# Kernel optimization log

Hardware: AMD Instinct MI355X
Metric: run time of the kernel (lower is better)

The kernel has to match this reference:

```python
import jax, jax.numpy as jnp
import numpy as np
from jax import lax

T, B, H_IN, H_HID = 2048, 64, 256, 256


def _orth(key, shape):
    a = jax.random.normal(key, shape, jnp.float32)
    if shape[0] >= shape[1]:
        q, _ = jnp.linalg.qr(a)
    else:
        q, _ = jnp.linalg.qr(a.T)
        q = q.T
    return q[: shape[0], : shape[1]].astype(jnp.float32)


def setup_inputs() -> dict:
    key = jax.random.key(0)
    ks = jax.random.split(key, 6)
    x = jax.random.normal(ks[0], (T, B, H_IN), jnp.float32)
    rnn_hxs = jax.random.normal(ks[1], (1, B, H_HID), jnp.float32)
    batch_mask = jax.random.randint(ks[2], (T, B), 0, 2).astype(bool)
    # force column 0 fully valid so pad_packed max length == T (static shape)
    batch_mask = batch_mask.at[:, 0].set(True)
    w_ih = _orth(ks[3], (3 * H_HID, H_IN))   # [3H, H_in] gates r,z,n
    w_hh = _orth(ks[4], (3 * H_HID, H_HID))
    b_ih = jnp.zeros((3 * H_HID,), jnp.float32)  # constant_(0) init
    b_hh = jnp.zeros((3 * H_HID,), jnp.float32)
    return {"x": x, "rnn_hxs": rnn_hxs, "batch_mask": batch_mask,
            "w_ih": w_ih, "w_hh": w_hh, "b_ih": b_ih, "b_hh": b_hh}


def _gru_ragged(x, h0, batch_mask, w_ih, w_hh, b_ih, b_hh):
    Tn, Bn, _ = x.shape
    Hh = h0.shape[-1]
    mask = batch_mask
    lens = mask.sum(0)                      # [B] per-column valid lengths
    # --- gather/pack: move valid steps of each column to the front ---
    rank = jnp.cumsum(mask, axis=0) - mask  # compact position per (t,b)
    rank_m = jnp.where(mask, rank, Tn)      # invalid rows -> dump row Tn
    cols = jnp.broadcast_to(jnp.arange(Bn), (Tn, Bn))
    compact = jnp.zeros((Tn + 1, Bn, x.shape[-1]), x.dtype)
    compact = compact.at[rank_m, cols].set(x)[:Tn]
    # --- GRU over compact sequences; h frozen past each column's length ---
    gi = jnp.einsum('tbi,gi->tbg', compact, w_ih) + b_ih  # [T,B,3H]
    valid = jnp.arange(Tn)[:, None] < lens[None, :]       # [T,B]

    def step(h, inp):
        gi_t, v = inp
        gh = jnp.einsum('bh,gh->bg', h, w_hh) + b_hh
        r = jax.nn.sigmoid(gi_t[:, :Hh] + gh[:, :Hh])
        z = jax.nn.sigmoid(gi_t[:, Hh:2 * Hh] + gh[:, Hh:2 * Hh])
        n = jnp.tanh(gi_t[:, 2 * Hh:] + r * gh[:, 2 * Hh:])
        h_new = (1.0 - z) * n + z * h
        h_out = jnp.where(v[:, None], h_new, h)
        out = jnp.where(v[:, None], h_new, 0.0)  # pad_packed zero padding
        return h_out, out

    hT, scores = lax.scan(step, h0, (gi, valid))  # scores [T,B,Hh]
    # --- masked_scatter: true positions of dest (row-major t,b order)
    # consume consecutive H-rows of the flattened padded scores ---
    mflat = mask.reshape(-1)
    flat_rank = jnp.cumsum(mflat) - mflat            # exclusive cumsum
    src = scores.reshape(Tn * Bn, Hh)
    gathered = src[flat_rank]                        # [T*B, Hh]
    out = jnp.where(mflat[:, None], gathered, 0.0).reshape(Tn, Bn, Hh)
    return out, hT


def reference(x, rnn_hxs, batch_mask, w_ih, w_hh, b_ih, b_hh):
    scores, hT = _gru_ragged(x, rnn_hxs[0], batch_mask, w_ih, w_hh, b_ih, b_hh)
    return scores, hT[None]
```

## Files before the change

kernel.cpp:

```cpp
#include <hip/hip_runtime.h>
#include <cstdint>
#include <cstddef>

#define T_LEN 2048
#define B_N   64
#define H_INP 256
#define H_HID 256
#define G3    768
#define M_ROWS (T_LEN * B_N)
#define SCH   16

typedef _Float16 f16;
typedef _Float16 f16x2 __attribute__((ext_vector_type(2)));
typedef _Float16 f16x8 __attribute__((ext_vector_type(8)));
typedef float    f32x4 __attribute__((ext_vector_type(4)));

__global__ void k_zero(float4* __restrict__ p, int n4) {
  int i = blockIdx.x * blockDim.x + threadIdx.x;
  int stride = gridDim.x * blockDim.x;
  float4 z; z.x = z.y = z.z = z.w = 0.f;
  for (; i < n4; i += stride) p[i] = z;
}

__global__ void k_cvt(const float2* __restrict__ s, f16x2* __restrict__ d, int n2) {
  int i = blockIdx.x * blockDim.x + threadIdx.x;
  int stride = gridDim.x * blockDim.x;
  for (; i < n2; i += stride) {
    float2 v = s[i];
    f16x2 p; p.x = (f16)v.x; p.y = (f16)v.y;
    d[i] = p;
  }
}

__global__ __launch_bounds__(64) void k_prep_col(const int* __restrict__ mask,
                                                 unsigned short* __restrict__ tidx,
                                                 int* __restrict__ lens) {
  const int b = blockIdx.x;
  const int lane = threadIdx.x;
  unsigned short* tp = tidx + b * T_LEN;
  int base = 0;
  for (int c = 0; c < T_LEN / 64; ++c) {
    int t = c * 64 + lane;
    bool m = mask[t * B_N + b] != 0;
    unsigned long long bal = __ballot(m);
    int pc = __popcll(bal & ((1ull << lane) - 1ull));
    if (m) tp[base + pc] = (unsigned short)t;
    base += __popcll(bal);
  }
  if (lane == 0) lens[b] = base;
}

__global__ __launch_bounds__(256) void k_rowcnt(const int* __restrict__ mask,
                                                int* __restrict__ rowcnt) {
  int g = blockIdx.x * 256 + threadIdx.x;
  int t = g >> 6, lane = g & 63;
  bool m = mask[t * B_N + lane] != 0;
  unsigned long long bal = __ballot(m);
  if (lane == 0) rowcnt[t] = __popcll(bal);
}

__global__ __launch_bounds__(512) void k_rowpref(const int* __restrict__ rowcnt,
                                                 int* __restrict__ rowpref,
                                                 int* __restrict__ ntru) {
  const int tid = threadIdx.x;
  const int lane = tid & 63, w = tid >> 6;
  int4 v = ((const int4*)rowcnt)[tid];
  int s = v.x + v.y + v.z + v.w;
  int incl = s;
  for (int d = 1; d < 64; d <<= 1) {
    int t = __shfl_up(incl, d, 64);
    if (lane >= d) incl += t;
  }
  __shared__ int wt[8], wo[8];
  if (lane == 63) wt[w] = incl;
  __syncthreads();
  if (tid == 0) {
    int run = 0;
    for (int i = 0; i < 8; ++i) { wo[i] = run; run += wt[i]; }
    ntru[0] = run;
  }
  __syncthreads();
  int base = wo[w] + incl - s;
  int4 o; o.x = base; o.y = base + v.x; o.z = o.y + v.y; o.w = o.z + v.z;
  ((int4*)rowpref)[tid] = o;
}

__global__ __launch_bounds__(256) void k_inv(const int* __restrict__ mask,
                                             const int* __restrict__ rowpref,
                                             int* __restrict__ inv) {
  int g = blockIdx.x * 256 + threadIdx.x;
  int t = g >> 6, lane = g & 63;
  bool m = mask[t * B_N + lane] != 0;
  unsigned long long bal = __ballot(m);
  int r = rowpref[t] + __popcll(bal & ((1ull << lane) - 1ull));
  if (m) inv[r] = t * B_N + lane;
}

__global__ __launch_bounds__(256) void k_gemm(const f16* __restrict__ X,
                                              const f16* __restrict__ W,
                                              const float* __restrict__ bias,
                                              f16* __restrict__ GI) {
  const int lane = threadIdx.x & 63;
  const int wave = threadIdx.x >> 6;
  const int m0 = blockIdx.x * 64 + wave * 16;
  const int n0 = blockIdx.y * 64;
  const int idx16 = lane & 15;
  const int kofs  = (lane >> 4) * 8;

  const f16* ap  = X + (size_t)(m0 + idx16) * H_INP + kofs;
  const f16* bp0 = W + (size_t)(n0 + idx16) * H_INP + kofs;

  f32x4 acc[4] = { {0,0,0,0}, {0,0,0,0}, {0,0,0,0}, {0,0,0,0} };
#pragma unroll
  for (int kt = 0; kt < 8; ++kt) {
    f16x8 a = *(const f16x8*)(ap + kt * 32);
#pragma unroll
    for (int nt = 0; nt < 4; ++nt) {
      f16x8 bb = *(const f16x8*)(bp0 + (size_t)nt * 16 * H_INP + kt * 32);
      acc[nt] = __builtin_amdgcn_mfma_f32_16x16x32_f16(a, bb, acc[nt], 0, 0, 0);
    }
  }
  const int mbase = m0 + (lane >> 4) * 4;
#pragma unroll
  for (int nt = 0; nt < 4; ++nt) {
    const int col = n0 + nt * 16 + idx16;
    const float bv = bias[col];
#pragma unroll
    for (int r = 0; r < 4; ++r)
      GI[(size_t)(mbase + r) * G3 + col] = (f16)(acc[nt][r] + bv);
  }
}

__global__ __launch_bounds__(768) void k_scan(const f16* __restrict__ Whh,
                                              const f16* __restrict__ GI,
                                              const float* __restrict__ h0,
                                              const float* __restrict__ bhh,
                                              const unsigned short* __restrict__ tidx,
                                              const int* __restrict__ lens,
                                              const int* __restrict__ inv,
                                              const int* __restrict__ ntru,
                                              float* __restrict__ out) {
  const int b = blockIdx.x;
  const int tid = threadIdx.x;
  const int lane = tid & 63;
  const int wav = tid >> 6;

  __shared__ f16   GIbuf[SCH * G3];
  __shared__ float outb[SCH * H_HID];
  __shared__ float ghs[G3];
  __shared__ f16   hpk[H_HID];
  __shared__ int   ivb[2][SCH];

  f16x8 bf[4][8];
  {
    const f16* wbase = Whh + (size_t)(wav * 64 + (lane & 15)) * H_HID + ((lane >> 4) << 3);
#pragma unroll
    for (int nt = 0; nt < 4; ++nt)
#pragma unroll
      for (int kc = 0; kc < 8; ++kc)
        bf[nt][kc] = *(const f16x8*)(wbase + (size_t)nt * 16 * H_HID + kc * 32);
  }
  float br = 0.f, bz = 0.f, bn = 0.f, h_reg = 0.f;
  if (tid < H_HID) {
    br = bhh[tid]; bz = bhh[H_HID + tid]; bn = bhh[2 * H_HID + tid];
    h_reg = h0[b * H_HID + tid];
  }
  if (tid < H_HID / 2) {
    float2 hv = ((const float2*)(h0 + b * H_HID))[tid];
    f16x2 p; p.x = (f16)hv.x; p.y = (f16)hv.y;
    ((f16x2*)hpk)[tid] = p;
  }
  const int L  = lens[b];
  const int Nt = ntru[0];
  const unsigned short* tptr = tidx + b * T_LEN;
  const bool arow = (lane & 15) == 0;
  const int  q = lane >> 4;

  for (int k = 0; k < L; ++k) {
    if ((k & (SCH - 1)) == 0) {
      const int par = (k >> 4) & 1;
      if (k > 0) {
        for (int r = wav; r < SCH; r += 12) {
          int iv = ivb[par ^ 1][r];
          if (iv >= 0)
            *(float4*)(out + (size_t)iv * H_HID + (lane << 2)) =
                *(const float4*)(outb + r * H_HID + (lane << 2));
        }
      }
      {
        int nrows = L - k; if (nrows > SCH) nrows = SCH;
        int r = tid / 48, c = tid % 48;
        if (r < nrows) {
          int t = tptr[k + r];
          const uint4* src = (const uint4*)(GI + ((size_t)t * B_N + b) * G3) + (c << 1);
          uint4 v0 = src[0], v1 = src[1];
          uint4* dst = (uint4*)(GIbuf + r * G3) + (c << 1);
          dst[0] = v0; dst[1] = v1;
        }
        if (tid < SCH) {
          int kk = k + tid;
          int pr = kk * B_N + b;
          ivb[par][tid] = (kk < L && pr < Nt) ? inv[pr] : -1;
        }
      }
      __syncthreads();
    }
    {
      const f32x4 z4 = {0.f, 0.f, 0.f, 0.f};
      f16x8 af = {0, 0, 0, 0, 0, 0, 0, 0};
      if (arow) af = *(const f16x8*)(hpk + (q << 3));
      f32x4 a0 = __builtin_amdgcn_mfma_f32_16x16x32_f16(af, bf[0][0], z4, 0, 0, 0);
      f32x4 a1 = __builtin_amdgcn_mfma_f32_16x16x32_f16(af, bf[1][0], z4, 0, 0, 0);
      f32x4 a2 = __builtin_amdgcn_mfma_f32_16x16x32_f16(af, bf[2][0], z4, 0, 0, 0);
      f32x4 a3 = __builtin_amdgcn_mfma_f32_16x16x32_f16(af, bf[3][0], z4, 0, 0, 0);
#pragma unroll
      for (int kc = 1; kc < 8; ++kc) {
        f16x8 a = {0, 0, 0, 0, 0, 0, 0, 0};
        if (arow) a = *(const f16x8*)(hpk + kc * 32 + (q << 3));
        a0 = __builtin_amdgcn_mfma_f32_16x16x32_f16(a, bf[0][kc], a0, 0, 0, 0);
        a1 = __builtin_amdgcn_mfma_f32_16x16x32_f16(a, bf[1][kc], a1, 0, 0, 0);
        a2 = __builtin_amdgcn_mfma_f32_16x16x32_f16(a, bf[2][kc], a2, 0, 0, 0);
        a3 = __builtin_amdgcn_mfma_f32_16x16x32_f16(a, bf[3][kc], a3, 0, 0, 0);
      }
      if (lane < 16) {
        float* g = ghs + wav * 64 + lane;
        g[0]  = a0[0];
        g[16] = a1[0];
        g[32] = a2[0];
        g[48] = a3[0];
      }
    }
    __syncthreads();
    if (tid < H_HID) {
      const int slot = k & (SCH - 1);
      const float gi0 = (float)GIbuf[slot * G3 + tid];
      const float gi1 = (float)GIbuf[slot * G3 + H_HID + tid];
      const float gi2 = (float)GIbuf[slot * G3 + 2 * H_HID + tid];
      const float ghr = ghs[tid] + br;
      const float ghz = ghs[H_HID + tid] + bz;
      const float ghn = ghs[2 * H_HID + tid] + bn;
      const float rg = __builtin_amdgcn_rcpf(1.f + __expf(-(gi0 + ghr)));
      const float zg = __builtin_amdgcn_rcpf(1.f + __expf(-(gi1 + ghz)));
      const float xx = gi2 + rg * ghn;
      const float ng = 1.f - 2.f * __builtin_amdgcn_rcpf(1.f + __expf(2.f * xx));
      const float hn = (1.f - zg) * ng + zg * h_reg;
      h_reg = hn;
      hpk[tid] = (f16)hn;
      outb[slot * H_HID + tid] = hn;
    }
    __syncthreads();
  }
  if (L > 0) {
    const int kb = (L - 1) & ~(SCH - 1);
    const int rows = L - kb;
    const int par = (kb >> 4) & 1;
    for (int r = wav; r < rows; r += 12) {
      int iv = ivb[par][r];
      if (iv >= 0)
        *(float4*)(out + (size_t)iv * H_HID + (lane << 2)) =
            *(const float4*)(outb + r * H_HID + (lane << 2));
    }
  }
  if (tid < H_HID)
    out[(size_t)M_ROWS * H_HID + (size_t)b * H_HID + tid] = h_reg;
}

extern "C" void kernel_launch(void* const* d_in, const int* in_sizes, int n_in,
                              void* d_out, int out_size, void* d_ws, size_t ws_size,
                              hipStream_t stream) {
  const float* x    = (const float*)d_in[0];
  const float* h0   = (const float*)d_in[1];
  const int*   mask = (const int*)d_in[2];
  const float* wih  = (const float*)d_in[3];
  const float* whh  = (const float*)d_in[4];
  const float* bih  = (const float*)d_in[5];
  const float* bhh  = (const float*)d_in[6];
  float* out = (float*)d_out;

  char* ws = (char*)d_ws;
  f16* X16   = (f16*)(ws + 0);
  f16* Wih16 = (f16*)(ws + 67108864);
  f16* Whh16 = (f16*)(ws + 67502080);
  f16* GI    = (f16*)(ws + 67895296);
  unsigned short* tidx = (unsigned short*)(ws + 269221888);
  int* rowcnt  = (int*)(ws + 269484032);
  int* rowpref = (int*)(ws + 269492224);
  int* inv   = (int*)(ws + 269746176);
  int* lens  = (int*)(ws + 270270464);
  int* ntru  = (int*)(ws + 270270720);

  hipLaunchKernelGGL(k_zero, dim3(4096), dim3(256), 0, stream,
                     (float4*)d_out, out_size / 4);
  hipLaunchKernelGGL(k_cvt, dim3(4096), dim3(256), 0, stream,
                     (const float2*)x, (f16x2*)X16, M_ROWS * H_INP / 2);
  hipLaunchKernelGGL(k_cvt, dim3(96), dim3(256), 0, stream,
                     (const float2*)wih, (f16x2*)Wih16, G3 * H_INP / 2);
  hipLaunchKernelGGL(k_cvt, dim3(96), dim3(256), 0, stream,
                     (const float2*)whh, (f16x2*)Whh16, G3 * H_INP / 2);
  hipLaunchKernelGGL(k_prep_col, dim3(B_N), dim3(64), 0, stream,
                     mask, tidx, lens);
  hipLaunchKernelGGL(k_rowcnt, dim3(512), dim3(256), 0, stream, mask, rowcnt);
  hipLaunchKernelGGL(k_rowpref, dim3(1), dim3(512), 0, stream,
                     rowcnt, rowpref, ntru);
  hipLaunchKernelGGL(k_inv, dim3(512), dim3(256), 0, stream,
                     mask, rowpref, inv);
  hipLaunchKernelGGL(k_gemm, dim3(M_ROWS / 64, G3 / 64), dim3(256), 0, stream,
                     X16, Wih16, bih, GI);
  hipLaunchKernelGGL(k_scan, dim3(B_N), dim3(768), 0, stream,
                     Whh16, GI, h0, bhh, tidx, lens, inv, ntru, out);
}
```

Before: 3.220 ms.

## Replace per-step MFMA recurrent matvec with register-resident fdot2 dot products

New measurement: 3.310 ms. 1.03x slower.

```diff
diff --git a/kernel.cpp b/kernel.cpp
--- a/kernel.cpp
+++ b/kernel.cpp
@@ -14,6 +14,17 @@
 typedef _Float16 f16x2 __attribute__((ext_vector_type(2)));
 typedef _Float16 f16x8 __attribute__((ext_vector_type(8)));
 typedef float    f32x4 __attribute__((ext_vector_type(4)));
+
+static __device__ __forceinline__ float fdot2f(uint32_t a, uint32_t b, float c) {
+#if __has_builtin(__builtin_amdgcn_fdot2)
+  return __builtin_amdgcn_fdot2(__builtin_bit_cast(f16x2, a),
+                                __builtin_bit_cast(f16x2, b), c, false);
+#else
+  f16x2 av = __builtin_bit_cast(f16x2, a);
+  f16x2 bv = __builtin_bit_cast(f16x2, b);
+  return c + (float)av.x * (float)bv.x + (float)av.y * (float)bv.y;
+#endif
+}
 
 __global__ void k_zero(float4* __restrict__ p, int n4) {
   int i = blockIdx.x * blockDim.x + threadIdx.x;
@@ -131,15 +142,15 @@
   }
 }
 
-__global__ __launch_bounds__(768) void k_scan(const f16* __restrict__ Whh,
-                                              const f16* __restrict__ GI,
-                                              const float* __restrict__ h0,
-                                              const float* __restrict__ bhh,
-                                              const unsigned short* __restrict__ tidx,
-                                              const int* __restrict__ lens,
-                                              const int* __restrict__ inv,
-                                              const int* __restrict__ ntru,
-                                              float* __restrict__ out) {
+__global__ __launch_bounds__(768, 3) void k_scan(const f16* __restrict__ Whh,
+                                                 const f16* __restrict__ GI,
+                                                 const float* __restrict__ h0,
+                                                 const float* __restrict__ bhh,
+                                                 const unsigned short* __restrict__ tidx,
+                                                 const int* __restrict__ lens,
+                                                 const int* __restrict__ inv,
+                                                 const int* __restrict__ ntru,
+                                                 float* __restrict__ out) {
   const int b = blockIdx.x;
   const int tid = threadIdx.x;
   const int lane = tid & 63;
@@ -147,24 +158,22 @@
 
   __shared__ f16   GIbuf[SCH * G3];
   __shared__ float outb[SCH * H_HID];
-  __shared__ float ghs[G3];
+  __shared__ float ghs[2 * H_HID];
   __shared__ f16   hpk[H_HID];
   __shared__ int   ivb[2][SCH];
 
-  f16x8 bf[4][8];
+  uint32_t w[128];
   {
-    const f16* wbase = Whh + (size_t)(wav * 64 + (lane & 15)) * H_HID + ((lane >> 4) << 3);
-#pragma unroll
-    for (int nt = 0; nt < 4; ++nt)
-#pragma unroll
-      for (int kc = 0; kc < 8; ++kc)
-        bf[nt][kc] = *(const f16x8*)(wbase + (size_t)nt * 16 * H_HID + kc * 32);
-  }
-  float br = 0.f, bz = 0.f, bn = 0.f, h_reg = 0.f;
-  if (tid < H_HID) {
-    br = bhh[tid]; bz = bhh[H_HID + tid]; bn = bhh[2 * H_HID + tid];
-    h_reg = h0[b * H_HID + tid];
-  }
+    const uint4* wp = (const uint4*)(Whh + (size_t)tid * H_HID);
+#pragma unroll
+    for (int i = 0; i < 32; ++i) {
+      uint4 v = wp[i];
+      w[4*i+0] = v.x; w[4*i+1] = v.y; w[4*i+2] = v.z; w[4*i+3] = v.w;
+    }
+  }
+  const float bias = bhh[tid];
+  float h_reg = 0.f;
+  if (tid < H_HID) h_reg = h0[b * H_HID + tid];
   if (tid < H_HID / 2) {
     float2 hv = ((const float2*)(h0 + b * H_HID))[tid];
     f16x2 p; p.x = (f16)hv.x; p.y = (f16)hv.y;
@@ -173,8 +182,7 @@
   const int L  = lens[b];
   const int Nt = ntru[0];
   const unsigned short* tptr = tidx + b * T_LEN;
-  const bool arow = (lane & 15) == 0;
-  const int  q = lane >> 4;
+  __syncthreads();
 
   for (int k = 0; k < L; ++k) {
     if ((k & (SCH - 1)) == 0) {
@@ -205,41 +213,37 @@
       }
       __syncthreads();
     }
+    float acc0 = bias, acc1 = 0.f;
     {
-      const f32x4 z4 = {0.f, 0.f, 0.f, 0.f};
-      f16x8 af = {0, 0, 0, 0, 0, 0, 0, 0};
-      if (arow) af = *(const f16x8*)(hpk + (q << 3));
-      f32x4 a0 = __builtin_amdgcn_mfma_f32_16x16x32_f16(af, bf[0][0], z4, 0, 0, 0);
-      f32x4 a1 = __builtin_amdgcn_mfma_f32_16x16x32_f16(af, bf[1][0], z4, 0, 0, 0);
-      f32x4 a2 = __builtin_amdgcn_mfma_f32_16x16x32_f16(af, bf[2][0], z4, 0, 0, 0);
-      f32x4 a3 = __builtin_amdgcn_mfma_f32_16x16x32_f16(af, bf[3][0], z4, 0, 0, 0);
-#pragma unroll
-      for (int kc = 1; kc < 8; ++kc) {
-        f16x8 a = {0, 0, 0, 0, 0, 0, 0, 0};
-        if (arow) a = *(const f16x8*)(hpk + kc * 32 + (q << 3));
-        a0 = __builtin_amdgcn_mfma_f32_16x16x32_f16(a, bf[0][kc], a0, 0, 0, 0);
-        a1 = __builtin_amdgcn_mfma_f32_16x16x32_f16(a, bf[1][kc], a1, 0, 0, 0);
-        a2 = __builtin_amdgcn_mfma_f32_16x16x32_f16(a, bf[2][kc], a2, 0, 0, 0);
-        a3 = __builtin_amdgcn_mfma_f32_16x16x32_f16(a, bf[3][kc], a3, 0, 0, 0);
+      const uint4* hb = (const uint4*)hpk;
+#pragma unroll
+      for (int i = 0; i < 16; ++i) {
+        uint4 hv = hb[i];
+        acc0 = fdot2f(w[4*i+0], hv.x, acc0);
+        acc0 = fdot2f(w[4*i+1], hv.y, acc0);
+        acc0 = fdot2f(w[4*i+2], hv.z, acc0);
+        acc0 = fdot2f(w[4*i+3], hv.w, acc0);
       }
-      if (lane < 16) {
-        float* g = ghs + wav * 64 + lane;
-        g[0]  = a0[0];
-        g[16] = a1[0];
-        g[32] = a2[0];
-        g[48] = a3[0];
+#pragma unroll
+      for (int i = 16; i < 32; ++i) {
+        uint4 hv = hb[i];
+        acc1 = fdot2f(w[4*i+0], hv.x, acc1);
+        acc1 = fdot2f(w[4*i+1], hv.y, acc1);
+        acc1 = fdot2f(w[4*i+2], hv.z, acc1);
+        acc1 = fdot2f(w[4*i+3], hv.w, acc1);
       }
     }
+    const float gh = acc0 + acc1;
+    if (tid >= H_HID) ghs[tid - H_HID] = gh;
     __syncthreads();
     if (tid < H_HID) {
       const int slot = k & (SCH - 1);
       const float gi0 = (float)GIbuf[slot * G3 + tid];
       const float gi1 = (float)GIbuf[slot * G3 + H_HID + tid];
       const float gi2 = (float)GIbuf[slot * G3 + 2 * H_HID + tid];
-      const float ghr = ghs[tid] + br;
-      const float ghz = ghs[H_HID + tid] + bz;
-      const float ghn = ghs[2 * H_HID + tid] + bn;
-      const float rg = __builtin_amdgcn_rcpf(1.f + __expf(-(gi0 + ghr)));
+      const float ghz = ghs[tid];
+      const float ghn = ghs[H_HID + tid];
+      const float rg = __builtin_amdgcn_rcpf(1.f + __expf(-(gi0 + gh)));
       const float zg = __builtin_amdgcn_rcpf(1.f + __expf(-(gi1 + ghz)));
       const float xx = gi2 + rg * ghn;
       const float ng = 1.f - 2.f * __builtin_amdgcn_rcpf(1.f + __expf(2.f * xx));
```
